# Optimization experiments

Measured on AMD Instinct MI355X. Metric: run time of the kernel, lower is better.

## Reference

```python
import jax, jax.numpy as jnp
import numpy as np

B, S, D = 2, 2048, 1024
H = 16
DK = D // H  # attn_dim // num_heads = 64
DV = D // H  # embed_dim // num_heads = 64
NEG = -1e9


def setup_inputs() -> dict:
    key = jax.random.key(0)
    ks = jax.random.split(key, 6)
    inputs = jax.random.normal(ks[0], (B, S, D), dtype=jnp.float32)
    # mask[b, i, j]: key position i may attend to query position j when i <= j (causal)
    mask = jnp.broadcast_to(jnp.triu(jnp.ones((S, S), dtype=bool))[None], (B, S, S))
    sd = 1.0 / np.sqrt(D)
    WQ = jax.random.normal(ks[1], (D, H, DK), dtype=jnp.float32) * sd
    WK = jax.random.normal(ks[2], (D, H, DK), dtype=jnp.float32) * sd
    WV = jax.random.normal(ks[3], (D, H, DV), dtype=jnp.float32) * sd
    WO = jax.random.normal(ks[4], (D, D), dtype=jnp.float32) * sd
    bO = jnp.zeros((D,), dtype=jnp.float32)
    return {"inputs": inputs, "mask": mask, "WQ": WQ, "WK": WK, "WV": WV, "WO": WO, "bO": bO}


def reference(inputs, mask, WQ, WK, WV, WO, bO):
    scale = 1.0 / jnp.sqrt(jnp.float32(DK))
    q = jnp.einsum('bid,dhk->bihk', inputs, WQ) * scale
    k = jnp.einsum('bid,dhk->bihk', inputs, WK)
    v = jnp.einsum('bid,dhv->bihv', inputs, WV)
    # scores: [b, i, j, h]; softmax over axis=1 (key axis i), as in the original
    scores = jnp.einsum('bihd,bjhd->bijh', q, k)
    scores = jnp.where(mask[..., None], scores, NEG)
    attn = jax.nn.softmax(scores, axis=1)
    x = jnp.einsum('bijh,bihv->bjhv', attn, v)  # output indexed by query j
    x = x.reshape(B, S, D)
    return x @ WO + bO
```

## Files before the change

### kernel.cpp

```cpp
#include <hip/hip_runtime.h>
#include <hip/hip_bf16.h>


typedef __bf16 bf16;
typedef __bf16 bf16x8 __attribute__((ext_vector_type(8)));
typedef __bf16 bf16x4 __attribute__((ext_vector_type(4)));
typedef float  f32x4  __attribute__((ext_vector_type(4)));

constexpr int Sq = 2048;
constexpr int Dm = 1024;
constexpr int Hh = 16;

#define KSCALE 0.18033688011112042f

static __device__ __forceinline__ void gload_lds16(const bf16* g, bf16* l) {
  __builtin_amdgcn_global_load_lds(
      (const __attribute__((address_space(1))) unsigned int*)g,
      (__attribute__((address_space(3))) unsigned int*)l, 16, 0, 0);
}

__global__ __launch_bounds__(256) void prep(
    const float* __restrict__ inputs,
    const float* __restrict__ WQ, const float* __restrict__ WK,
    const float* __restrict__ WV, const float* __restrict__ WO,
    bf16* __restrict__ Xin, bf16* __restrict__ Wt) {
  __shared__ bf16 t[64][65];
  const int bx = blockIdx.x;
  const int tid = threadIdx.x;
  if (bx < 2048) {
    const int i = (bx * 256 + tid) * 8;
    float4 a = *reinterpret_cast<const float4*>(inputs + i);
    float4 b = *reinterpret_cast<const float4*>(inputs + i + 4);
    bf16x8 o;
    o[0] = (bf16)a.x; o[1] = (bf16)a.y; o[2] = (bf16)a.z; o[3] = (bf16)a.w;
    o[4] = (bf16)b.x; o[5] = (bf16)b.y; o[6] = (bf16)b.z; o[7] = (bf16)b.w;
    *reinterpret_cast<bf16x8*>(Xin + i) = o;
    return;
  }
  const int rr0 = bx - 2048;
  const int z = rr0 >> 8;
  const int tt = rr0 & 255;
  const int r0 = (tt >> 4) * 64, c0 = (tt & 15) * 64;
  const float* in = (z == 0) ? WQ : (z == 1) ? WK : (z == 2) ? WV : WO;
  bf16* op = Wt + (size_t)z * 1024 * 1024;
  const int rr = tid >> 3, cc = (tid & 7) * 8;
#pragma unroll
  for (int it = 0; it < 2; ++it) {
    int row = rr + it * 32;
    const float* ip = in + (size_t)(r0 + row) * 1024 + c0 + cc;
    float4 a = *reinterpret_cast<const float4*>(ip);
    float4 b = *reinterpret_cast<const float4*>(ip + 4);
    t[row][cc + 0] = (bf16)a.x; t[row][cc + 1] = (bf16)a.y;
    t[row][cc + 2] = (bf16)a.z; t[row][cc + 3] = (bf16)a.w;
    t[row][cc + 4] = (bf16)b.x; t[row][cc + 5] = (bf16)b.y;
    t[row][cc + 6] = (bf16)b.z; t[row][cc + 7] = (bf16)b.w;
  }
  __syncthreads();
#pragma unroll
  for (int it = 0; it < 2; ++it) {
    int crow = rr + it * 32;
    alignas(16) bf16 o[8];
#pragma unroll
    for (int e = 0; e < 8; ++e) o[e] = t[cc + e][crow];
    *reinterpret_cast<bf16x8*>(op + (size_t)(c0 + crow) * 1024 + r0 + cc) =
        *reinterpret_cast<bf16x8*>(o);
  }
}

template <int EPI, int MT>
__global__ __launch_bounds__(256) void gemm128(
    const bf16* __restrict__ A, const bf16* __restrict__ Bt,
    const int M, const int N, const int K,
    bf16* __restrict__ Katt, bf16* __restrict__ Qatt, bf16* __restrict__ VattT,
    const float* __restrict__ bOf, float* __restrict__ Cout) {
  constexpr int MF = MT / 32;
  __shared__ bf16 As[MT * 64], Bs[8192];
  const int tid = threadIdx.x;
  const int lane = tid & 63;
  const int w = tid >> 6;
  const int wr = w >> 1, wc = w & 1;
  const int g = lane >> 4, c = lane & 15;
  const int m0 = blockIdx.y * MT, n0 = blockIdx.x * 128;
  const int sr = lane >> 3;
  const int scp = ((lane & 7) ^ sr) * 8;

  f32x4 acc[MF][4];
#pragma unroll
  for (int i = 0; i < MF; ++i)
#pragma unroll
    for (int j = 0; j < 4; ++j) acc[i][j] = f32x4{0.f, 0.f, 0.f, 0.f};

  for (int k0 = 0; k0 < K; k0 += 64) {
#pragma unroll
    for (int p = 0; p < MT / 32; ++p) {
      const int rowb = p * 32 + w * 8;
      gload_lds16(A + (size_t)(m0 + rowb + sr) * K + k0 + scp, &As[rowb * 64]);
    }
#pragma unroll
    for (int p = 0; p < 4; ++p) {
      const int rowb = p * 32 + w * 8;
      gload_lds16(Bt + (size_t)(n0 + rowb + sr) * K + k0 + scp, &Bs[rowb * 64]);
    }
    __syncthreads();
#pragma unroll
    for (int kk = 0; kk < 2; ++kk) {
      const int ch = kk * 4 + g;
      bf16x8 af[MF], bfr[4];
#pragma unroll
      for (int mf = 0; mf < MF; ++mf) {
        const int row = wr * (MT / 2) + mf * 16 + c;
        af[mf] = *reinterpret_cast<const bf16x8*>(
            &As[row * 64 + ((ch ^ (row & 7)) << 3)]);
      }
#pragma unroll
      for (int nf = 0; nf < 4; ++nf) {
        const int row = wc * 64 + nf * 16 + c;
        bfr[nf] = *reinterpret_cast<const bf16x8*>(
            &Bs[row * 64 + ((ch ^ (row & 7)) << 3)]);
      }
#pragma unroll
      for (int mf = 0; mf < MF; ++mf)
#pragma unroll
        for (int nf = 0; nf < 4; ++nf)
          acc[mf][nf] = __builtin_amdgcn_mfma_f32_16x16x32_bf16(
              af[mf], bfr[nf], acc[mf][nf], 0, 0, 0);
    }
    __syncthreads();
  }

#pragma unroll
  for (int mf = 0; mf < MF; ++mf)
#pragma unroll
    for (int nf = 0; nf < 4; ++nf) {
      const int n = n0 + wc * 64 + nf * 16 + c;
      const int mb = m0 + wr * (MT / 2) + mf * 16 + g * 4;
      if (EPI == 0 && n >= 2048) {
        bf16x4 pk;
#pragma unroll
        for (int r = 0; r < 4; ++r) pk[r] = (bf16)acc[mf][nf][r];
        const int b = mb >> 11, sb = mb & (Sq - 1);
        const int h = (n >> 6) & 15, dk = n & 63;
        *reinterpret_cast<bf16x4*>(
            &VattT[((size_t)(b * Hh + h) * 64 + dk) * Sq + sb]) = pk;
      } else {
#pragma unroll
        for (int r = 0; r < 4; ++r) {
          const int m = mb + r;
          float v = acc[mf][nf][r];
          if (EPI == 0) {
            const int b = m >> 11, s = m & (Sq - 1);
            const int h = (n >> 6) & 15, dk = n & 63;
            const int bh = b * Hh + h;
            if (n < 1024)
              Katt[((size_t)bh * Sq + s) * 64 + dk] = (bf16)(v * KSCALE);
            else
              Qatt[((size_t)bh * Sq + s) * 64 + dk] = (bf16)v;
          } else {
            Cout[(size_t)m * N + n] = v + bOf[n];
          }
        }
      }
    }
}

__global__ __launch_bounds__(256, 2) void attn_v7(
    const bf16* __restrict__ Q, const bf16* __restrict__ K,
    const bf16* __restrict__ Vt, bf16* __restrict__ X) {
  __shared__ bf16 Kb[2][4096];
  __shared__ bf16 Vb[2][4096];
  __shared__ bf16 Pb[8192];
  const int tid = threadIdx.x, lane = tid & 63, w = tid >> 6;
  const int g = lane >> 4, c = lane & 15;
  const int bx = blockIdx.x;
  const int u = bx >> 5;
  const int bh = bx & 31;
  const int um = (u + 4 * (bh >> 3)) & 15;
  const int qblk = (um < 8) ? um : 23 - um;
  const int b = bh >> 4, h = bh & 15;
  const size_t base = (size_t)bh * Sq * 64;
  const bf16* Kg = K + base;
  const bf16* Vg = Vt + (size_t)bh * 64 * Sq;
  const int trow = tid >> 3, tch = tid & 7;

  bf16x8 qf[2][2];
#pragma unroll
  for (int z = 0; z < 2; ++z) {
    const bf16* Qg = Q + base + ((size_t)qblk * 128 + z * 64 + w * 16 + c) * 64;
    qf[z][0] = *reinterpret_cast<const bf16x8*>(Qg + g * 8);
    qf[z][1] = *reinterpret_cast<const bf16x8*>(Qg + 32 + g * 8);
  }

#pragma unroll
  for (int pp = 0; pp < 2; ++pp) {
    int row = trow + pp * 32;
    *reinterpret_cast<bf16x8*>(&Kb[0][row * 64 + ((tch ^ (row & 7)) << 3)]) =
        *reinterpret_cast<const bf16x8*>(Kg + (size_t)row * 64 + tch * 8);
    *reinterpret_cast<bf16x8*>(&Vb[0][row * 64 + ((tch ^ (row & 7)) << 3)]) =
        *reinterpret_cast<const bf16x8*>(Vg + (size_t)row * Sq + tch * 8);
  }
  __syncthreads();

  f32x4 acc[2][4];
  float lpart[2][4];
#pragma unroll
  for (int z = 0; z < 2; ++z)
#pragma unroll
    for (int r = 0; r < 4; ++r) {
      lpart[z][r] = 0.f;
      acc[z][r] = f32x4{0.f, 0.f, 0.f, 0.f};
    }

  const int ntiles = 2 * qblk + 2;
  for (int t = 0; t < ntiles; ++t) {
    const int cur = t & 1;
    const bf16* Kc = Kb[cur];
    const bf16* Vc = Vb[cur];
    const bool hasnext = (t + 1 < ntiles);
    const bool act0 = (t != ntiles - 1);

    bf16x8 kr0, kr1, vr0, vr1;
    if (hasnext) {
      const int i1 = (t + 1) * 64;
      kr0 = *reinterpret_cast<const bf16x8*>(Kg + (size_t)(i1 + trow) * 64 + tch * 8);
      kr1 = *reinterpret_cast<const bf16x8*>(Kg + (size_t)(i1 + trow + 32) * 64 + tch * 8);
      vr0 = *reinterpret_cast<const bf16x8*>(Vg + (size_t)trow * Sq + i1 + tch * 8);
      vr1 = *reinterpret_cast<const bf16x8*>(Vg + (size_t)(trow + 32) * Sq + i1 + tch * 8);
    }

    f32x4 sc[2][4];
#pragma unroll
    for (int z = 0; z < 2; ++z)
#pragma unroll
      for (int kg = 0; kg < 4; ++kg) sc[z][kg] = f32x4{0.f, 0.f, 0.f, 0.f};
#pragma unroll
    for (int kk = 0; kk < 2; ++kk) {
      const int ch = kk * 4 + g;
      bf16x8 kf[4];
#pragma unroll
      for (int kg = 0; kg < 4; ++kg) {
        int row = kg * 16 + c;
        kf[kg] = *reinterpret_cast<const bf16x8*>(
            &Kc[row * 64 + ((ch ^ (row & 7)) << 3)]);
      }
#pragma unroll
      for (int kg = 0; kg < 4; ++kg) {
        sc[1][kg] = __builtin_amdgcn_mfma_f32_16x16x32_bf16(
            qf[1][kk], kf[kg], sc[1][kg], 0, 0, 0);
        if (act0)
          sc[0][kg] = __builtin_amdgcn_mfma_f32_16x16x32_bf16(
              qf[0][kk], kf[kg], sc[0][kg], 0, 0, 0);
      }
    }

#pragma unroll
    for (int z = 0; z < 2; ++z) {
      if (z == 0 && !act0) continue;
      const bool diag = (z == 0) ? (t == ntiles - 2) : (t == ntiles - 1);
      bf16* Pz = Pb + (size_t)(w * 2 + z) * 1024;
#pragma unroll
      for (int kg = 0; kg < 4; ++kg)
#pragma unroll
        for (int r = 0; r < 4; ++r) {
          float p = __builtin_amdgcn_exp2f(sc[z][kg][r]);
          if (diag) {
            const int i = t * 64 + kg * 16 + c;
            const int j = qblk * 128 + z * 64 + w * 16 + g * 4 + r;
            p = (i <= j) ? p : 0.f;
          }
          lpart[z][r] += p;
          const int prow = g * 4 + r, pcol = kg * 16 + c;
          Pz[prow * 64 + (((pcol >> 3) ^ (prow & 7)) << 3) + (pcol & 7)] = (bf16)p;
        }
    }

#pragma unroll
    for (int ks = 0; ks < 2; ++ks) {
      const int ch = ks * 4 + g;
      bf16x8 pf1 = *reinterpret_cast<const bf16x8*>(
          &Pb[(size_t)(w * 2 + 1) * 1024 + c * 64 + ((ch ^ (c & 7)) << 3)]);
      bf16x8 pf0;
      if (act0)
        pf0 = *reinterpret_cast<const bf16x8*>(
            &Pb[(size_t)(w * 2 + 0) * 1024 + c * 64 + ((ch ^ (c & 7)) << 3)]);
#pragma unroll
      for (int vg = 0; vg < 4; ++vg) {
        int dv = vg * 16 + c;
        bf16x8 vf = *reinterpret_cast<const bf16x8*>(
            &Vc[dv * 64 + ((ch ^ (dv & 7)) << 3)]);
        acc[1][vg] = __builtin_amdgcn_mfma_f32_16x16x32_bf16(
            pf1, vf, acc[1][vg], 0, 0, 0);
        if (act0)
          acc[0][vg] = __builtin_amdgcn_mfma_f32_16x16x32_bf16(
              pf0, vf, acc[0][vg], 0, 0, 0);
      }
    }

    if (hasnext) {
      bf16* Kn = Kb[cur ^ 1];
      bf16* Vn = Vb[cur ^ 1];
      const int row0 = trow, row1 = trow + 32;
      *reinterpret_cast<bf16x8*>(&Kn[row0 * 64 + ((tch ^ (row0 & 7)) << 3)]) = kr0;
      *reinterpret_cast<bf16x8*>(&Kn[row1 * 64 + ((tch ^ (row1 & 7)) << 3)]) = kr1;
      *reinterpret_cast<bf16x8*>(&Vn[row0 * 64 + ((tch ^ (row0 & 7)) << 3)]) = vr0;
      *reinterpret_cast<bf16x8*>(&Vn[row1 * 64 + ((tch ^ (row1 & 7)) << 3)]) = vr1;
    }
    __syncthreads();
  }

#pragma unroll
  for (int z = 0; z < 2; ++z) {
    float linv[4];
#pragma unroll
    for (int r = 0; r < 4; ++r) {
      float l = lpart[z][r];
      l += __shfl_xor(l, 1);
      l += __shfl_xor(l, 2);
      l += __shfl_xor(l, 4);
      l += __shfl_xor(l, 8);
      linv[r] = 1.f / l;
    }
#pragma unroll
    for (int vg = 0; vg < 4; ++vg)
#pragma unroll
      for (int r = 0; r < 4; ++r) {
        const int j = qblk * 128 + z * 64 + w * 16 + g * 4 + r;
        const int dv = vg * 16 + c;
        X[((size_t)b * Sq + j) * Dm + h * 64 + dv] = (bf16)(acc[z][vg][r] * linv[r]);
      }
  }
}

extern "C" void kernel_launch(void* const* d_in, const int* in_sizes, int n_in,
                              void* d_out, int out_size, void* d_ws, size_t ws_size,
                              hipStream_t stream) {
  const float* inputs = (const float*)d_in[0];
  const float* WQ = (const float*)d_in[2];
  const float* WK = (const float*)d_in[3];
  const float* WV = (const float*)d_in[4];
  const float* WO = (const float*)d_in[5];
  const float* bO = (const float*)d_in[6];
  float* out = (float*)d_out;

  bf16* Xin   = (bf16*)d_ws;
  bf16* Wt    = Xin + 4096 * 1024;
  bf16* Katt  = Wt + 4 * 1024 * 1024;
  bf16* Qatt  = Katt + (1 << 22);
  bf16* VattT = Qatt + (1 << 22);
  bf16* X     = Xin;

  prep<<<3072, 256, 0, stream>>>(inputs, WQ, WK, WV, WO, Xin, Wt);

  gemm128<0, 128><<<dim3(24, 32), 256, 0, stream>>>(
      Xin, Wt, 4096, 3072, 1024, Katt, Qatt, VattT, nullptr, nullptr);

  attn_v7<<<dim3(512), 256, 0, stream>>>(Qatt, Katt, VattT, X);

  gemm128<1, 64><<<dim3(8, 64), 256, 0, stream>>>(
      X, Wt + 3 * 1024 * 1024, 4096, 1024, 1024,
      nullptr, nullptr, nullptr, bO, out);
}
```

Baseline: 103.7 us.

## Keep attention probabilities in registers by transposing the QK MFMA operands

Swaps the A/B operands of the score MFMA so each lane holds S^T values whose layout matches the A-operand layout of the PV MFMA. The probabilities are packed straight into bf16x8 registers instead of going through a 16 KB shared-memory P buffer, which removes the LDS writes and reads and cuts shared memory use. V fragments are now gathered with two 4-element LDS reads per MFMA to match the new k ordering, and the row-sum reduction is reworked to use cross-group shuffles. The risk is more LDS read instructions for V and extra register packing work.

```diff
diff --git a/kernel.cpp b/kernel.cpp
--- a/kernel.cpp
+++ b/kernel.cpp
@@ -163,12 +163,11 @@
     }
 }
 
-__global__ __launch_bounds__(256, 2) void attn_v7(
+__global__ __launch_bounds__(256, 2) void attn_v11(
     const bf16* __restrict__ Q, const bf16* __restrict__ K,
     const bf16* __restrict__ Vt, bf16* __restrict__ X) {
   __shared__ bf16 Kb[2][4096];
   __shared__ bf16 Vb[2][4096];
-  __shared__ bf16 Pb[8192];
   const int tid = threadIdx.x, lane = tid & 63, w = tid >> 6;
   const int g = lane >> 4, c = lane & 15;
   const int bx = blockIdx.x;
@@ -201,14 +200,11 @@
   __syncthreads();
 
   f32x4 acc[2][4];
-  float lpart[2][4];
+  float lpart[2] = {0.f, 0.f};
 #pragma unroll
   for (int z = 0; z < 2; ++z)
 #pragma unroll
-    for (int r = 0; r < 4; ++r) {
-      lpart[z][r] = 0.f;
-      acc[z][r] = f32x4{0.f, 0.f, 0.f, 0.f};
-    }
+    for (int vg = 0; vg < 4; ++vg) acc[z][vg] = f32x4{0.f, 0.f, 0.f, 0.f};
 
   const int ntiles = 2 * qblk + 2;
   for (int t = 0; t < ntiles; ++t) {
@@ -245,53 +241,68 @@
 #pragma unroll
       for (int kg = 0; kg < 4; ++kg) {
         sc[1][kg] = __builtin_amdgcn_mfma_f32_16x16x32_bf16(
-            qf[1][kk], kf[kg], sc[1][kg], 0, 0, 0);
+            kf[kg], qf[1][kk], sc[1][kg], 0, 0, 0);
         if (act0)
           sc[0][kg] = __builtin_amdgcn_mfma_f32_16x16x32_bf16(
-              qf[0][kk], kf[kg], sc[0][kg], 0, 0, 0);
-      }
-    }
-
+              kf[kg], qf[0][kk], sc[0][kg], 0, 0, 0);
+      }
+    }
+
+    bf16x4 pa[2][4];
 #pragma unroll
     for (int z = 0; z < 2; ++z) {
       if (z == 0 && !act0) continue;
       const bool diag = (z == 0) ? (t == ntiles - 2) : (t == ntiles - 1);
-      bf16* Pz = Pb + (size_t)(w * 2 + z) * 1024;
+      const int j = qblk * 128 + z * 64 + w * 16 + c;
 #pragma unroll
       for (int kg = 0; kg < 4; ++kg)
 #pragma unroll
         for (int r = 0; r < 4; ++r) {
-          float p = __builtin_amdgcn_exp2f(sc[z][kg][r]);
+          float pv = __builtin_amdgcn_exp2f(sc[z][kg][r]);
           if (diag) {
-            const int i = t * 64 + kg * 16 + c;
-            const int j = qblk * 128 + z * 64 + w * 16 + g * 4 + r;
-            p = (i <= j) ? p : 0.f;
+            const int i = t * 64 + kg * 16 + g * 4 + r;
+            pv = (i <= j) ? pv : 0.f;
           }
-          lpart[z][r] += p;
-          const int prow = g * 4 + r, pcol = kg * 16 + c;
-          Pz[prow * 64 + (((pcol >> 3) ^ (prow & 7)) << 3) + (pcol & 7)] = (bf16)p;
+          lpart[z] += pv;
+          pa[z][kg][r] = (bf16)pv;
         }
     }
 
 #pragma unroll
     for (int ks = 0; ks < 2; ++ks) {
-      const int ch = ks * 4 + g;
-      bf16x8 pf1 = *reinterpret_cast<const bf16x8*>(
-          &Pb[(size_t)(w * 2 + 1) * 1024 + c * 64 + ((ch ^ (c & 7)) << 3)]);
-      bf16x8 pf0;
-      if (act0)
-        pf0 = *reinterpret_cast<const bf16x8*>(
-            &Pb[(size_t)(w * 2 + 0) * 1024 + c * 64 + ((ch ^ (c & 7)) << 3)]);
+      bf16x8 pa1, pa0;
+#pragma unroll
+      for (int e = 0; e < 4; ++e) {
+        pa1[e] = pa[1][2 * ks][e];
+        pa1[4 + e] = pa[1][2 * ks + 1][e];
+      }
+      if (act0) {
+#pragma unroll
+        for (int e = 0; e < 4; ++e) {
+          pa0[e] = pa[0][2 * ks][e];
+          pa0[4 + e] = pa[0][2 * ks + 1][e];
+        }
+      }
 #pragma unroll
       for (int vg = 0; vg < 4; ++vg) {
-        int dv = vg * 16 + c;
-        bf16x8 vf = *reinterpret_cast<const bf16x8*>(
-            &Vc[dv * 64 + ((ch ^ (dv & 7)) << 3)]);
+        const int dv = vg * 16 + c;
+        const int ko0 = 32 * ks + 4 * g;
+        const int ko1 = ko0 + 16;
+        bf16x4 v0 = *reinterpret_cast<const bf16x4*>(
+            &Vc[dv * 64 + (((ko0 >> 3) ^ (dv & 7)) << 3) + (ko0 & 7)]);
+        bf16x4 v1 = *reinterpret_cast<const bf16x4*>(
+            &Vc[dv * 64 + (((ko1 >> 3) ^ (dv & 7)) << 3) + (ko1 & 7)]);
+        bf16x8 vfr;
+#pragma unroll
+        for (int e = 0; e < 4; ++e) {
+          vfr[e] = v0[e];
+          vfr[4 + e] = v1[e];
+        }
         acc[1][vg] = __builtin_amdgcn_mfma_f32_16x16x32_bf16(
-            pf1, vf, acc[1][vg], 0, 0, 0);
+            pa1, vfr, acc[1][vg], 0, 0, 0);
         if (act0)
           acc[0][vg] = __builtin_amdgcn_mfma_f32_16x16x32_bf16(
-              pf0, vf, acc[0][vg], 0, 0, 0);
+              pa0, vfr, acc[0][vg], 0, 0, 0);
       }
     }
 
@@ -309,16 +320,13 @@
 
 #pragma unroll
   for (int z = 0; z < 2; ++z) {
+    float l = lpart[z];
+    l += __shfl_xor(l, 16);
+    l += __shfl_xor(l, 32);
     float linv[4];
 #pragma unroll
-    for (int r = 0; r < 4; ++r) {
-      float l = lpart[z][r];
-      l += __shfl_xor(l, 1);
-      l += __shfl_xor(l, 2);
-      l += __shfl_xor(l, 4);
-      l += __shfl_xor(l, 8);
-      linv[r] = 1.f / l;
-    }
+    for (int r = 0; r < 4; ++r)
+      linv[r] = 1.f / __shfl(l, g * 4 + r);
 #pragma unroll
     for (int vg = 0; vg < 4; ++vg)
 #pragma unroll
@@ -353,7 +361,7 @@
   gemm128<0, 128><<<dim3(24, 32), 256, 0, stream>>>(
       Xin, Wt, 4096, 3072, 1024, Katt, Qatt, VattT, nullptr, nullptr);
 
-  attn_v7<<<dim3(512), 256, 0, stream>>>(Qatt, Katt, VattT, X);
+  attn_v11<<<dim3(512), 256, 0, stream>>>(Qatt, Katt, VattT, X);
 
   gemm128<1, 64><<<dim3(8, 64), 256, 0, stream>>>(
       X, Wt + 3 * 1024 * 1024, 4096, 1024, 1024,
```

Measured after the change: 100.0 us. 1.04x faster.
